# Kernel optimization log

Hardware: AMD Instinct MI355X
Metric: run time of the kernel (lower is better)

Reference implementation:

```python
import jax, jax.numpy as jnp
import numpy as np
import math

HID = 1024   # hidden_dim
QKV = 1024   # qkv_dim
H = 16       # num_heads
DH = QKV // H  # head_dim = 64
BS = 16      # block_size
EPS = 1e-12


def setup_inputs() -> dict:
    key = jax.random.key(0)
    ks = jax.random.split(key, 6)
    B, L = 2, 4096
    s = 0.02
    return {
        "q": jax.random.normal(ks[0], (B, L, HID), jnp.float32),
        "Wq": jax.random.normal(ks[1], (HID, QKV), jnp.float32) * s,
        "Wk": jax.random.normal(ks[2], (HID, QKV), jnp.float32) * s,
        "Wv": jax.random.normal(ks[3], (HID, QKV), jnp.float32) * s,
        "Wo": jax.random.normal(ks[4], (QKV, HID), jnp.float32) * s,
        "bo": jnp.zeros((HID,), jnp.float32),
    }


def _swap_pairs(xb):
    # xb: [B,H,n_blocks,BS,D] -> swap adjacent block pairs along n_blocks
    b, h, n, bs, d = xb.shape
    x = xb.reshape(b, h, n // 2, 2, bs, d)[:, :, :, ::-1]
    return x.reshape(b, h, n, bs, d)


def _block_attend(qb, kb, vb, scale):
    # qb,kb,vb: [B,H,n,BS,D]. Un-normalized block attention (masks are all-ones
    # -> additive mask term is 0). Returns per-block y and row-sum A.
    logits = jnp.einsum('bhnqd,bhnkd->bhnqk', qb * scale, kb)
    logits = logits - jnp.max(logits, axis=-1, keepdims=True)
    A = jnp.exp(logits)
    y = jnp.einsum('bhnqk,bhnkd->bhnqd', A, vb)
    return y, A.sum(axis=-1)


def _to_blocks(x):
    b, h, l, d = x.shape
    return x.reshape(b, h, l // BS, BS, d)


def _forward(q, Wq, Wk, Wv, Wo, bo):
    B, L, _ = q.shape  # L is a power of 2 (4096), no padding needed
    Q, K, V = q @ Wq, q @ Wk, q @ Wv
    sh = lambda x: x.reshape(B, L, H, DH).transpose(0, 2, 1, 3)  # [B,H,L,D]
    Q, K, V = sh(Q), sh(K), sh(V)
    scale = 1.0 / math.sqrt(DH)
    num_levels = int(math.log2(L // BS)) - 1  # 7 for L=4096

    # Multi-level coarsening: avg-pool q/k, sum-pool v (masks all-ones)
    levels = [(Q, K, V)]
    cq, ck, cv = Q, K, V
    for _ in range(num_levels):
        pool = lambda x, red: red(x.reshape(B, H, x.shape[2] // 2, 2, DH), axis=3)
        cq = pool(cq, jnp.mean)
        ck = pool(ck, jnp.mean)
        cv = pool(cv, jnp.sum)
        levels.append((cq, ck, cv))

    # Coarsest-to-finest: block attention against swapped neighbor blocks,
    # repeat-interleave accumulator by 2 at each finer level and add.
    y, A = None, None
    for cq, ck, cv in reversed(levels):
        qb = _to_blocks(cq)
        kb = _swap_pairs(_to_blocks(ck))
        vb = _swap_pairs(_to_blocks(cv))
        yl, Al = _block_attend(qb, kb, vb, scale)
        yl = yl.reshape(B, H, -1, DH)
        Al = Al.reshape(B, H, -1)
        if y is None:
            y, A = yl, Al
        else:
            y = jnp.repeat(y, 2, axis=2) + yl
            A = jnp.repeat(A, 2, axis=2) + Al

    # Finest diagonal blocks, no swap
    yl, Al = _block_attend(_to_blocks(Q), _to_blocks(K), _to_blocks(V), scale)
    y = y + yl.reshape(B, H, L, DH)
    A = A + Al.reshape(B, H, L)

    out = y / (A + EPS)[..., None]
    out = out.transpose(0, 2, 1, 3).reshape(B, L, H * DH)
    return out @ Wo + bo


def reference(q, Wq, Wk, Wv, Wo, bo):
    return _forward(q, Wq, Wk, Wv, Wo, bo)
```

## Files before the change

### kernel.cpp

```cpp
#include <hip/hip_runtime.h>
#include <cstddef>
#include <cstdint>

#define NHEADS 16
#define DHEAD  64
#define SEQL   4096
#define NBH    32
#define PBH_POOL 4064

typedef unsigned short bfu;
typedef unsigned int u32;
typedef __attribute__((ext_vector_type(4)))  float f32x4;
typedef __attribute__((ext_vector_type(16))) float f32x16;
typedef __attribute__((ext_vector_type(8)))  short bf16x8;

__device__ inline float b2f(bfu b) { return __uint_as_float(((unsigned)b) << 16); }
__device__ inline bfu f2b(float f) {
    unsigned u = __float_as_uint(f);
    unsigned r = 0x7FFFu + ((u >> 16) & 1u);
    return (bfu)((u + r) >> 16);
}
__device__ inline u32 pk2(float a, float b) {
    return (u32)f2b(a) | ((u32)f2b(b) << 16);
}
__device__ inline bf16x8 mk8(u32 a, u32 b, u32 c, u32 d) {
    union { u32 u[4]; bf16x8 v; } x;
    x.u[0] = a; x.u[1] = b; x.u[2] = c; x.u[3] = d;
    return x.v;
}

__global__ __launch_bounds__(256) void cvt_q(const float* __restrict__ q, bfu* __restrict__ qb)
{
    size_t g = (size_t)blockIdx.x * 256 + threadIdx.x;
    float4 v = *reinterpret_cast<const float4*>(&q[g * 4]);
    ushort4 s;
    s.x = f2b(v.x); s.y = f2b(v.y); s.z = f2b(v.z); s.w = f2b(v.w);
    *reinterpret_cast<ushort4*>(&qb[g * 4]) = s;
}

__global__ __launch_bounds__(256) void transpose_cvt(
    const float* __restrict__ W0, const float* __restrict__ W1,
    const float* __restrict__ W2, const float* __restrict__ W3,
    bfu* __restrict__ Wt)
{
    __shared__ float t[32][33];
    const int widx = blockIdx.z;
    const float* src = (widx == 0) ? W0 : (widx == 1) ? W1 : (widx == 2) ? W2 : W3;
    bfu* dst = Wt + (size_t)widx * 1048576;
    const int k0 = blockIdx.y * 32, n0 = blockIdx.x * 32;
    const int tx = threadIdx.x & 31, ty = threadIdx.x >> 5;
    #pragma unroll
    for (int i = 0; i < 4; ++i)
        t[ty + 8 * i][tx] = src[(size_t)(k0 + ty + 8 * i) * 1024 + n0 + tx];
    __syncthreads();
    #pragma unroll
    for (int i = 0; i < 4; ++i)
        dst[(size_t)(n0 + ty + 8 * i) * 1024 + k0 + tx] = f2b(t[tx][ty + 8 * i]);
}

template<int MODE>
__global__ __launch_bounds__(256) void gemm_mfma(
    const bfu* __restrict__ A, const bfu* __restrict__ Bt,
    bfu* __restrict__ O0, bfu* __restrict__ O1, bfu* __restrict__ O2,
    float* __restrict__ Ofp, const float* __restrict__ bias)
{
    __shared__ bfu As[128 * 32];
    __shared__ bfu Bs[128 * 32];
    const int tid = threadIdx.x;
    const int lane = tid & 63;
    const int wv = tid >> 6;
    const int wr = wv >> 1, wc = wv & 1;
    const int m0 = blockIdx.y * 128, n0 = blockIdx.x * 128;
    const int rlo = lane & 15, khi = lane >> 4;

    f32x4 acc[4][4];
    #pragma unroll
    for (int i = 0; i < 4; ++i)
        #pragma unroll
        for (int j = 0; j < 4; ++j)
            #pragma unroll
            for (int e = 0; e < 4; ++e) acc[i][j][e] = 0.f;

    for (int kt = 0; kt < 1024; kt += 32) {
        #pragma unroll
        for (int r = 0; r < 2; ++r) {
            int o = (r * 256 + tid) * 16;
            int row = o >> 6;
            int slot = (o >> 4) & 3;
            int sg = slot ^ ((row >> 1) & 3);
            __builtin_amdgcn_global_load_lds(
                (const __attribute__((address_space(1))) u32*)
                    &A[(size_t)(m0 + row) * 1024 + kt + sg * 8],
                (__attribute__((address_space(3))) u32*)
                    (reinterpret_cast<char*>(As) + o), 16, 0, 0);
            __builtin_amdgcn_global_load_lds(
                (const __attribute__((address_space(1))) u32*)
                    &Bt[(size_t)(n0 + row) * 1024 + kt + sg * 8],
                (__attribute__((address_space(3))) u32*)
                    (reinterpret_cast<char*>(Bs) + o), 16, 0, 0);
        }
        __syncthreads();
        bf16x8 af[4], bf_[4];
        #pragma unroll
        for (int mf = 0; mf < 4; ++mf) {
            int row = wr * 64 + mf * 16 + rlo;
            af[mf] = *reinterpret_cast<const bf16x8*>(
                reinterpret_cast<char*>(As) + row * 64 + ((khi ^ ((row >> 1) & 3)) << 4));
        }
        #pragma unroll
        for (int nf = 0; nf < 4; ++nf) {
            int row = wc * 64 + nf * 16 + rlo;
            bf_[nf] = *reinterpret_cast<const bf16x8*>(
                reinterpret_cast<char*>(Bs) + row * 64 + ((khi ^ ((row >> 1) & 3)) << 4));
        }
        #pragma unroll
        for (int mf = 0; mf < 4; ++mf)
            #pragma unroll
            for (int nf = 0; nf < 4; ++nf)
                acc[mf][nf] = __builtin_amdgcn_mfma_f32_16x16x32_bf16(
                    af[mf], bf_[nf], acc[mf][nf], 0, 0, 0);
        __syncthreads();
    }

    if (MODE == 0) {
        #pragma unroll
        for (int mf = 0; mf < 4; ++mf) {
            #pragma unroll
            for (int nf = 0; nf < 4; ++nf) {
                int np = n0 + wc * 64 + nf * 16 + rlo;
                int wsel = np >> 10, n = np & 1023;
                int h = n >> 6, d = n & 63;
                bfu* O = (wsel == 0) ? O0 : ((wsel == 1) ? O1 : O2);
                #pragma unroll
                for (int rr = 0; rr < 4; ++rr) {
                    int m = m0 + wr * 64 + mf * 16 + khi * 4 + rr;
                    int b = m >> 12, l = m & 4095;
                    O[(((size_t)(b * NHEADS + h)) * SEQL + l) * DHEAD + d] = f2b(acc[mf][nf][rr]);
                }
            }
        }
    } else {
        #pragma unroll
        for (int mf = 0; mf < 4; ++mf) {
            #pragma unroll
            for (int nf = 0; nf < 4; ++nf) {
                int np = n0 + wc * 64 + nf * 16 + rlo;
                float bb = bias[np];
                #pragma unroll
                for (int rr = 0; rr < 4; ++rr) {
                    int m = m0 + wr * 64 + mf * 16 + khi * 4 + rr;
                    Ofp[(size_t)m * 1024 + np] = acc[mf][nf][rr] + bb;
                }
            }
        }
    }
}

__global__ __launch_bounds__(256) void transpose_v(
    const bfu* __restrict__ Vb, bfu* __restrict__ Vt0)
{
    __shared__ bfu tile[64 * 64];
    const int bh = blockIdx.y, l0 = blockIdx.x * 64;
    const int t = threadIdx.x;
    const int row = t >> 3, chunk = t & 7;
    #pragma unroll
    for (int it = 0; it < 2; ++it) {
        int r = it * 32 + row;
        uint4 v = *reinterpret_cast<const uint4*>(
            &Vb[((size_t)bh * SEQL + l0 + r) * 64 + chunk * 8]);
        bfu e[8];
        e[0] = v.x & 0xffff; e[1] = v.x >> 16; e[2] = v.y & 0xffff; e[3] = v.y >> 16;
        e[4] = v.z & 0xffff; e[5] = v.z >> 16; e[6] = v.w & 0xffff; e[7] = v.w >> 16;
        int pr = r ^ (chunk * 8);
        #pragma unroll
        for (int j = 0; j < 8; ++j) tile[(chunk * 8 + j) * 64 + pr] = e[j];
    }
    __syncthreads();
    #pragma unroll
    for (int it = 0; it < 2; ++it) {
        int d = it * 32 + (t >> 3);
        int lc = t & 7;
        int plc = lc ^ (d >> 3);
        uint4 v = *reinterpret_cast<const uint4*>(&tile[d * 64 + plc * 8]);
        *reinterpret_cast<uint4*>(
            &Vt0[((size_t)bh * 64 + d) * SEQL + l0 + lc * 8]) = v;
    }
}

__global__ __launch_bounds__(256) void pool2x(
    const bfu* __restrict__ sq, const bfu* __restrict__ sk, const bfu* __restrict__ svt,
    bfu* __restrict__ dq, bfu* __restrict__ dk, bfu* __restrict__ dvt,
    int srcPerBH, int srcRow0, int dstRow0, int dstRows, int svtCols)
{
    int g = blockIdx.x * 256 + threadIdx.x;
    int half = NBH * dstRows * 16;
    if (g < half) {
        int per = dstRows * 16;
        int bh = g / per, f = g % per;
        int r = f >> 4, cc = (f & 15) * 4;
        size_t s0 = ((size_t)bh * srcPerBH + srcRow0 + 2 * r) * 64 + cc;
        size_t di = ((size_t)bh * PBH_POOL + dstRow0 + r) * 64 + cc;
        ushort4 a, b, o;
        a = *reinterpret_cast<const ushort4*>(&sq[s0]);
        b = *reinterpret_cast<const ushort4*>(&sq[s0 + 64]);
        o.x = f2b((b2f(a.x) + b2f(b.x)) * 0.5f);
        o.y = f2b((b2f(a.y) + b2f(b.y)) * 0.5f);
        o.z = f2b((b2f(a.z) + b2f(b.z)) * 0.5f);
        o.w = f2b((b2f(a.w) + b2f(b.w)) * 0.5f);
        *reinterpret_cast<ushort4*>(&dq[di]) = o;
        a = *reinterpret_cast<const ushort4*>(&sk[s0]);
        b = *reinterpret_cast<const ushort4*>(&sk[s0 + 64]);
        o.x = f2b((b2f(a.x) + b2f(b.x)) * 0.5f);
        o.y = f2b((b2f(a.y) + b2f(b.y)) * 0.5f);
        o.z = f2b((b2f(a.z) + b2f(b.z)) * 0.5f);
        o.w = f2b((b2f(a.w) + b2f(b.w)) * 0.5f);
        *reinterpret_cast<ushort4*>(&dk[di]) = o;
    } else {
        g -= half;
        int nr4 = dstRows >> 2;
        int per = 64 * nr4;
        int bh = g / per, f = g % per;
        int d = f / nr4, r4 = (f % nr4) * 4;
        const bfu* srow = svt + ((size_t)bh * 64 + d) * svtCols + srcRow0 + 2 * r4;
        uint4 v = *reinterpret_cast<const uint4*>(srow);
        ushort4 o;
        o.x = f2b(b2f(v.x & 0xffff) + b2f(v.x >> 16));
        o.y = f2b(b2f(v.y & 0xffff) + b2f(v.y >> 16));
        o.z = f2b(b2f(v.z & 0xffff) + b2f(v.z >> 16));
        o.w = f2b(b2f(v.w & 0xffff) + b2f(v.w >> 16));
        *reinterpret_cast<ushort4*>(&dvt[((size_t)bh * 64 + d) * PBH_POOL + dstRow0 + r4]) = o;
    }
}

__global__ __launch_bounds__(64) void pair_attn(
    const bfu* __restrict__ Q0, const bfu* __restrict__ K0, const bfu* __restrict__ Vt0,
    const bfu* __restrict__ Qp, const bfu* __restrict__ Kp, const bfu* __restrict__ Vtp,
    bfu* __restrict__ y0, float* __restrict__ A0,
    bfu* __restrict__ ylev, float* __restrict__ Alev)
{
    const int bh = blockIdx.y;
    int s = blockIdx.x, lvl = 0, cnt = 128;
    while (s >= cnt) { s -= cnt; cnt >>= 1; ++lvl; }
    const bfu *Q, *K, *Vt; int perbh, vcols, loff;
    if (lvl == 0) { Q = Q0; K = K0; Vt = Vt0; perbh = SEQL; vcols = SEQL; loff = 0; }
    else { Q = Qp; K = Kp; Vt = Vtp; perbh = PBH_POOL; vcols = PBH_POOL; loff = 4096 - (8192 >> lvl); }
    const int rbase = loff + s * 32;
    const int t = threadIdx.x, q31 = t & 31, hl = t >> 5;

    const bfu* Krow = K + ((size_t)bh * perbh + rbase + q31) * 64 + hl * 8;
    const bfu* Qrow = Q + ((size_t)bh * perbh + rbase + q31) * 64 + hl * 8;

    f32x16 S;
    #pragma unroll
    for (int e = 0; e < 16; ++e) S[e] = 0.f;
    #pragma unroll
    for (int db = 0; db < 4; ++db) {
        bf16x8 ka = *reinterpret_cast<const bf16x8*>(Krow + db * 16);
        bf16x8 qa = *reinterpret_cast<const bf16x8*>(Qrow + db * 16);
        S = __builtin_amdgcn_mfma_f32_32x32x16_bf16(ka, qa, S, 0, 0, 0);
    }

    float p[16];
    #pragma unroll
    for (int r = 0; r < 16; ++r) p[r] = S[r] * 0.125f;
    float mlo = p[0], mhi = p[8];
    #pragma unroll
    for (int r = 1; r < 8; ++r) { mlo = fmaxf(mlo, p[r]); mhi = fmaxf(mhi, p[r + 8]); }
    mlo = fmaxf(mlo, __shfl_xor(mlo, 32));
    mhi = fmaxf(mhi, __shfl_xor(mhi, 32));
    #pragma unroll
    for (int r = 0; r < 8; ++r) {
        p[r]     = __expf(p[r]     - mlo);
        p[r + 8] = __expf(p[r + 8] - mhi);
    }
    if (lvl > 0) {
        #pragma unroll
        for (int r = 0; r < 8; ++r) {
            if (q31 < 16) p[r] = 0.f; else p[r + 8] = 0.f;
        }
    }
    float alo = 0.f, ahi = 0.f;
    #pragma unroll
    for (int r = 0; r < 8; ++r) { alo += p[r]; ahi += p[r + 8]; }
    alo += __shfl_xor(alo, 32);
    ahi += __shfl_xor(ahi, 32);
    const float Asum = alo + ahi;

    bf16x8 Pop[2];
    #pragma unroll
    for (int m = 0; m < 2; ++m) {
        u32 a0 = pk2(p[8 * m + 0], p[8 * m + 1]);
        u32 a1 = pk2(p[8 * m + 2], p[8 * m + 3]);
        u32 b0 = pk2(p[8 * m + 4], p[8 * m + 5]);
        u32 b1 = pk2(p[8 * m + 6], p[8 * m + 7]);
        u32 pa0 = __shfl_xor(a0, 32), pa1 = __shfl_xor(a1, 32);
        u32 pb0 = __shfl_xor(b0, 32), pb1 = __shfl_xor(b1, 32);
        Pop[m] = (hl == 0) ? mk8(a0, a1, pa0, pa1) : mk8(pb0, pb1, b0, b1);
    }

    const bfu* Vbase = Vt + (size_t)bh * 64 * vcols + rbase + hl * 8;
    f32x16 y[2];
    #pragma unroll
    for (int tt = 0; tt < 2; ++tt) {
        #pragma unroll
        for (int e = 0; e < 16; ++e) y[tt][e] = 0.f;
        #pragma unroll
        for (int m = 0; m < 2; ++m) {
            bf16x8 va = *reinterpret_cast<const bf16x8*>(
                Vbase + (size_t)(tt * 32 + q31) * vcols + m * 16);
            y[tt] = __builtin_amdgcn_mfma_f32_32x32x16_bf16(va, Pop[m], y[tt], 0, 0, 0);
        }
    }

    if (lvl == 0) {
        const int b = bh >> 4, h = bh & 15;
        bfu* orow = y0 + ((size_t)(b * SEQL + rbase + q31)) * 1024 + h * 64;
        #pragma unroll
        for (int tt = 0; tt < 2; ++tt)
            #pragma unroll
            for (int g = 0; g < 4; ++g) {
                int d0 = tt * 32 + g * 8 + hl * 4;
                ushort4 s4;
                s4.x = f2b(y[tt][4 * g + 0]); s4.y = f2b(y[tt][4 * g + 1]);
                s4.z = f2b(y[tt][4 * g + 2]); s4.w = f2b(y[tt][4 * g + 3]);
                *reinterpret_cast<ushort4*>(orow + d0) = s4;
            }
        if (hl == 0) A0[(size_t)bh * SEQL + rbase + q31] = Asum;
    } else {
        bfu* orow = ylev + ((size_t)bh * PBH_POOL + rbase + q31) * 64;
        #pragma unroll
        for (int tt = 0; tt < 2; ++tt)
            #pragma unroll
            for (int g = 0; g < 4; ++g) {
                int d0 = tt * 32 + g * 8 + hl * 4;
                ushort4 s4;
                s4.x = f2b(y[tt][4 * g + 0]); s4.y = f2b(y[tt][4 * g + 1]);
                s4.z = f2b(y[tt][4 * g + 2]); s4.w = f2b(y[tt][4 * g + 3]);
                *reinterpret_cast<ushort4*>(orow + d0) = s4;
            }
        if (hl == 0) Alev[(size_t)bh * PBH_POOL + rbase + q31] = Asum;
    }
}

__global__ __launch_bounds__(256) void gather_norm(
    const bfu* __restrict__ ylev, const float* __restrict__ Alev,
    const float* __restrict__ A0, bfu* __restrict__ y0)
{
    size_t g = (size_t)blockIdx.x * 256 + threadIdx.x;
    int d = (int)(g & 63);
    int h = (int)((g >> 6) & 15);
    int l = (int)((g >> 10) & 4095);
    int b = (int)(g >> 22);
    int bh = b * NHEADS + h;

    float ys = b2f(y0[g]);
    float as = A0[(size_t)bh * SEQL + l];
    #pragma unroll
    for (int lvl = 1; lvl <= 7; ++lvl) {
        int r = (4096 - (8192 >> lvl)) + (l >> lvl);
        ys += b2f(ylev[((size_t)bh * PBH_POOL + r) * 64 + d]);
        as += Alev[(size_t)bh * PBH_POOL + r];
    }
    y0[g] = f2b(ys / (as + 1e-12f));
}

extern "C" void kernel_launch(void* const* d_in, const int* in_sizes, int n_in,
                              void* d_out, int out_size, void* d_ws, size_t ws_size,
                              hipStream_t stream)
{
    const float* q  = (const float*)d_in[0];
    const float* Wq = (const float*)d_in[1];
    const float* Wk = (const float*)d_in[2];
    const float* Wv = (const float*)d_in[3];
    const float* Wo = (const float*)d_in[4];
    const float* bo = (const float*)d_in[5];
    float* out = (float*)d_out;

    const size_t NE0 = (size_t)NBH * SEQL * 64;
    const size_t NEP = (size_t)NBH * PBH_POOL * 64;
    bfu* qb   = (bfu*)d_ws;
    bfu* Wt   = qb + NE0;
    bfu* Qb   = Wt + 4 * 1048576;
    bfu* Kb   = Qb + NE0;
    bfu* Vb   = Kb + NE0;
    bfu* Vt0  = Vb + NE0;
    bfu* Qp   = Vt0 + NE0;
    bfu* Kp   = Qp + NEP;
    bfu* ylev = Kp + NEP;
    float* Alev = (float*)(ylev + NEP);
    float* A0   = Alev + (size_t)NBH * PBH_POOL;
    bfu* Vtp  = Vb;

    cvt_q<<<8192, 256, 0, stream>>>(q, qb);
    transpose_cvt<<<dim3(32, 32, 4), 256, 0, stream>>>(Wq, Wk, Wv, Wo, Wt);

    gemm_mfma<0><<<dim3(24, 64), 256, 0, stream>>>(
        qb, Wt, Qb, Kb, Vb, nullptr, nullptr);

    transpose_v<<<dim3(64, NBH), 256, 0, stream>>>(Vb, Vt0);

    for (int lvl = 1; lvl < 8; ++lvl) {
        int Ld = 4096 >> lvl;
        int srcPerBH = (lvl == 1) ? SEQL : PBH_POOL;
        int srcRow0  = (lvl == 1) ? 0 : (4096 - (8192 >> (lvl - 1)));
        int dstRow0  = 4096 - (8192 >> lvl);
        const bfu* sq  = (lvl == 1) ? Qb : Qp;
        const bfu* sk  = (lvl == 1) ? Kb : Kp;
        const bfu* svt = (lvl == 1) ? Vt0 : Vtp;
        int svtCols    = (lvl == 1) ? SEQL : PBH_POOL;
        int nblk = (NBH * Ld * 32) / 256;
        pool2x<<<nblk, 256, 0, stream>>>(sq, sk, svt, Qp, Kp, Vtp,
                                         srcPerBH, srcRow0, dstRow0, Ld, svtCols);
    }

    pair_attn<<<dim3(255, NBH), 64, 0, stream>>>(
        Qb, Kb, Vt0, Qp, Kp, Vtp, qb , A0, ylev, Alev);

    gather_norm<<<32768, 256, 0, stream>>>(ylev, Alev, A0, qb);

    gemm_mfma<1><<<dim3(8, 64), 256, 0, stream>>>(
        qb, Wt + 3 * 1048576, nullptr, nullptr, nullptr, out, bo);
}
```

Baseline: 288.9 us.

## Fuse prep kernels, write V transposed from GEMM, single-pass pooling, vectorize gather

Merges the q conversion and weight transpose into one launch, and has the QKV GEMM epilogue write V directly in transposed layout, which removes the separate transpose_v kernel. The seven per-level pool launches become one kernel in which each block pools a 128-row segment through all levels in shared memory. pair_attn packs four 64-thread slots into each 256-thread block, and gather_norm handles four elements per thread with vector loads. This cuts launch count and global round-trips. Pooled levels are now computed in fp32 from the finest bf16 data rather than re-rounded at each level, and the pool kernel uses a large shared-memory footprint.

```diff
diff --git a/kernel.cpp b/kernel.cpp
--- a/kernel.cpp
+++ b/kernel.cpp
@@ -29,33 +29,36 @@
     return x.v;
 }
 
-__global__ __launch_bounds__(256) void cvt_q(const float* __restrict__ q, bfu* __restrict__ qb)
-{
-    size_t g = (size_t)blockIdx.x * 256 + threadIdx.x;
-    float4 v = *reinterpret_cast<const float4*>(&q[g * 4]);
-    ushort4 s;
-    s.x = f2b(v.x); s.y = f2b(v.y); s.z = f2b(v.z); s.w = f2b(v.w);
-    *reinterpret_cast<ushort4*>(&qb[g * 4]) = s;
-}
-
-__global__ __launch_bounds__(256) void transpose_cvt(
+__global__ __launch_bounds__(256) void prep(
+    const float* __restrict__ q,
     const float* __restrict__ W0, const float* __restrict__ W1,
     const float* __restrict__ W2, const float* __restrict__ W3,
-    bfu* __restrict__ Wt)
-{
-    __shared__ float t[32][33];
-    const int widx = blockIdx.z;
-    const float* src = (widx == 0) ? W0 : (widx == 1) ? W1 : (widx == 2) ? W2 : W3;
-    bfu* dst = Wt + (size_t)widx * 1048576;
-    const int k0 = blockIdx.y * 32, n0 = blockIdx.x * 32;
-    const int tx = threadIdx.x & 31, ty = threadIdx.x >> 5;
-    #pragma unroll
-    for (int i = 0; i < 4; ++i)
-        t[ty + 8 * i][tx] = src[(size_t)(k0 + ty + 8 * i) * 1024 + n0 + tx];
-    __syncthreads();
-    #pragma unroll
-    for (int i = 0; i < 4; ++i)
-        dst[(size_t)(n0 + ty + 8 * i) * 1024 + k0 + tx] = f2b(t[tx][ty + 8 * i]);
+    bfu* __restrict__ qb, bfu* __restrict__ Wt)
+{
+    const int bid = blockIdx.x;
+    if (bid < 8192) {
+        size_t g = (size_t)bid * 256 + threadIdx.x;
+        float4 v = *reinterpret_cast<const float4*>(&q[g * 4]);
+        ushort4 s;
+        s.x = f2b(v.x); s.y = f2b(v.y); s.z = f2b(v.z); s.w = f2b(v.w);
+        *reinterpret_cast<ushort4*>(&qb[g * 4]) = s;
+    } else {
+        __shared__ float tl[32][33];
+        const int b2 = bid - 8192;
+        const int widx = b2 >> 10;
+        const int tile = b2 & 1023;
+        const float* src = (widx == 0) ? W0 : (widx == 1) ? W1 : (widx == 2) ? W2 : W3;
+        bfu* dst = Wt + (size_t)widx * 1048576;
+        const int n0 = (tile & 31) * 32, k0 = (tile >> 5) * 32;
+        const int tx = threadIdx.x & 31, ty = threadIdx.x >> 5;
+        #pragma unroll
+        for (int i = 0; i < 4; ++i)
+            tl[ty + 8 * i][tx] = src[(size_t)(k0 + ty + 8 * i) * 1024 + n0 + tx];
+        __syncthreads();
+        #pragma unroll
+        for (int i = 0; i < 4; ++i)
+            dst[(size_t)(n0 + ty + 8 * i) * 1024 + k0 + tx] = f2b(tl[tx][ty + 8 * i]);
+    }
 }
 
 template<int MODE>
@@ -125,17 +128,25 @@
     if (MODE == 0) {
         #pragma unroll
         for (int mf = 0; mf < 4; ++mf) {
+            int l0m = m0 + wr * 64 + mf * 16 + khi * 4;
+            int b = l0m >> 12, l0 = l0m & 4095;
             #pragma unroll
             for (int nf = 0; nf < 4; ++nf) {
                 int np = n0 + wc * 64 + nf * 16 + rlo;
                 int wsel = np >> 10, n = np & 1023;
                 int h = n >> 6, d = n & 63;
-                bfu* O = (wsel == 0) ? O0 : ((wsel == 1) ? O1 : O2);
-                #pragma unroll
-                for (int rr = 0; rr < 4; ++rr) {
-                    int m = m0 + wr * 64 + mf * 16 + khi * 4 + rr;
-                    int b = m >> 12, l = m & 4095;
-                    O[(((size_t)(b * NHEADS + h)) * SEQL + l) * DHEAD + d] = f2b(acc[mf][nf][rr]);
+                if (wsel == 2) {
+                    ushort4 s4;
+                    s4.x = f2b(acc[mf][nf][0]); s4.y = f2b(acc[mf][nf][1]);
+                    s4.z = f2b(acc[mf][nf][2]); s4.w = f2b(acc[mf][nf][3]);
+                    *reinterpret_cast<ushort4*>(
+                        &O2[((size_t)(b * NHEADS + h) * 64 + d) * SEQL + l0]) = s4;
+                } else {
+                    bfu* O = (wsel == 0) ? O0 : O1;
+                    #pragma unroll
+                    for (int rr = 0; rr < 4; ++rr)
+                        O[(((size_t)(b * NHEADS + h)) * SEQL + l0 + rr) * DHEAD + d]
+                            = f2b(acc[mf][nf][rr]);
                 }
             }
         }
@@ -156,96 +167,107 @@
     }
 }
 
-__global__ __launch_bounds__(256) void transpose_v(
-    const bfu* __restrict__ Vb, bfu* __restrict__ Vt0)
-{
-    __shared__ bfu tile[64 * 64];
-    const int bh = blockIdx.y, l0 = blockIdx.x * 64;
+__global__ __launch_bounds__(256) void pool_all(
+    const bfu* __restrict__ Qb, const bfu* __restrict__ Kb, const bfu* __restrict__ Vt0,
+    bfu* __restrict__ Qp, bfu* __restrict__ Kp, bfu* __restrict__ Vtp)
+{
+    __shared__ bfu stg[8192];
+    __shared__ float buf0[4096];
+    __shared__ float buf1[4096];
+    const int bid = blockIdx.x;
     const int t = threadIdx.x;
-    const int row = t >> 3, chunk = t & 7;
-    #pragma unroll
-    for (int it = 0; it < 2; ++it) {
-        int r = it * 32 + row;
-        uint4 v = *reinterpret_cast<const uint4*>(
-            &Vb[((size_t)bh * SEQL + l0 + r) * 64 + chunk * 8]);
-        bfu e[8];
-        e[0] = v.x & 0xffff; e[1] = v.x >> 16; e[2] = v.y & 0xffff; e[3] = v.y >> 16;
-        e[4] = v.z & 0xffff; e[5] = v.z >> 16; e[6] = v.w & 0xffff; e[7] = v.w >> 16;
-        int pr = r ^ (chunk * 8);
-        #pragma unroll
-        for (int j = 0; j < 8; ++j) tile[(chunk * 8 + j) * 64 + pr] = e[j];
-    }
-    __syncthreads();
-    #pragma unroll
-    for (int it = 0; it < 2; ++it) {
-        int d = it * 32 + (t >> 3);
-        int lc = t & 7;
-        int plc = lc ^ (d >> 3);
-        uint4 v = *reinterpret_cast<const uint4*>(&tile[d * 64 + plc * 8]);
-        *reinterpret_cast<uint4*>(
-            &Vt0[((size_t)bh * 64 + d) * SEQL + l0 + lc * 8]) = v;
-    }
-}
-
-__global__ __launch_bounds__(256) void pool2x(
-    const bfu* __restrict__ sq, const bfu* __restrict__ sk, const bfu* __restrict__ svt,
-    bfu* __restrict__ dq, bfu* __restrict__ dk, bfu* __restrict__ dvt,
-    int srcPerBH, int srcRow0, int dstRow0, int dstRows, int svtCols)
-{
-    int g = blockIdx.x * 256 + threadIdx.x;
-    int half = NBH * dstRows * 16;
-    if (g < half) {
-        int per = dstRows * 16;
-        int bh = g / per, f = g % per;
-        int r = f >> 4, cc = (f & 15) * 4;
-        size_t s0 = ((size_t)bh * srcPerBH + srcRow0 + 2 * r) * 64 + cc;
-        size_t di = ((size_t)bh * PBH_POOL + dstRow0 + r) * 64 + cc;
-        ushort4 a, b, o;
-        a = *reinterpret_cast<const ushort4*>(&sq[s0]);
-        b = *reinterpret_cast<const ushort4*>(&sq[s0 + 64]);
-        o.x = f2b((b2f(a.x) + b2f(b.x)) * 0.5f);
-        o.y = f2b((b2f(a.y) + b2f(b.y)) * 0.5f);
-        o.z = f2b((b2f(a.z) + b2f(b.z)) * 0.5f);
-        o.w = f2b((b2f(a.w) + b2f(b.w)) * 0.5f);
-        *reinterpret_cast<ushort4*>(&dq[di]) = o;
-        a = *reinterpret_cast<const ushort4*>(&sk[s0]);
-        b = *reinterpret_cast<const ushort4*>(&sk[s0 + 64]);
-        o.x = f2b((b2f(a.x) + b2f(b.x)) * 0.5f);
-        o.y = f2b((b2f(a.y) + b2f(b.y)) * 0.5f);
-        o.z = f2b((b2f(a.z) + b2f(b.z)) * 0.5f);
-        o.w = f2b((b2f(a.w) + b2f(b.w)) * 0.5f);
-        *reinterpret_cast<ushort4*>(&dk[di]) = o;
+
+    if (bid < 2048) {
+        const int tensor = bid >> 10;
+        const int bh = (bid & 1023) >> 5, seg = bid & 31;
+        const bfu* src = (tensor ? Kb : Qb) + ((size_t)bh * SEQL + seg * 128) * 64;
+        bfu* dst = (tensor ? Kp : Qp) + (size_t)bh * PBH_POOL * 64;
+        #pragma unroll
+        for (int it = 0; it < 4; ++it) {
+            int tt = it * 256 + t;
+            *reinterpret_cast<uint4*>(&stg[(tt >> 3) * 64 + (tt & 7) * 8]) =
+                *reinterpret_cast<const uint4*>(&src[(size_t)(tt >> 3) * 64 + (tt & 7) * 8]);
+        }
+        __syncthreads();
+        {
+            int d = t & 63;
+            #pragma unroll
+            for (int i = 0; i < 16; ++i) {
+                int r = (t >> 6) + 4 * i;
+                float v = (b2f(stg[(2 * r) * 64 + d]) + b2f(stg[(2 * r + 1) * 64 + d])) * 0.5f;
+                buf0[r * 64 + d] = v;
+                dst[(size_t)(seg * 64 + r) * 64 + d] = f2b(v);
+            }
+        }
+        __syncthreads();
+        int nr = 32, dstRow0 = 2048;
+        float* cur = buf0; float* nxt = buf1;
+        for (int lvl = 2; lvl <= 7; ++lvl) {
+            int elems = nr * 64;
+            for (int i = t; i < elems; i += 256) {
+                int r = i >> 6, dd = i & 63;
+                float v = (cur[(2 * r) * 64 + dd] + cur[(2 * r + 1) * 64 + dd]) * 0.5f;
+                nxt[r * 64 + dd] = v;
+                dst[(size_t)(dstRow0 + seg * nr + r) * 64 + dd] = f2b(v);
+            }
+            __syncthreads();
+            float* tmp = cur; cur = nxt; nxt = tmp;
+            dstRow0 += 4096 >> lvl;
+            nr >>= 1;
+        }
     } else {
-        g -= half;
-        int nr4 = dstRows >> 2;
-        int per = 64 * nr4;
-        int bh = g / per, f = g % per;
-        int d = f / nr4, r4 = (f % nr4) * 4;
-        const bfu* srow = svt + ((size_t)bh * 64 + d) * svtCols + srcRow0 + 2 * r4;
-        uint4 v = *reinterpret_cast<const uint4*>(srow);
-        ushort4 o;
-        o.x = f2b(b2f(v.x & 0xffff) + b2f(v.x >> 16));
-        o.y = f2b(b2f(v.y & 0xffff) + b2f(v.y >> 16));
-        o.z = f2b(b2f(v.z & 0xffff) + b2f(v.z >> 16));
-        o.w = f2b(b2f(v.w & 0xffff) + b2f(v.w >> 16));
-        *reinterpret_cast<ushort4*>(&dvt[((size_t)bh * 64 + d) * PBH_POOL + dstRow0 + r4]) = o;
-    }
-}
-
-__global__ __launch_bounds__(64) void pair_attn(
+        const int b2 = bid - 2048;
+        const int bh = b2 >> 5, seg = b2 & 31;
+        const bfu* src = Vt0 + (size_t)bh * 64 * SEQL + seg * 128;
+        bfu* dst = Vtp + (size_t)bh * 64 * PBH_POOL;
+        #pragma unroll
+        for (int it = 0; it < 4; ++it) {
+            int tt = it * 256 + t;
+            *reinterpret_cast<uint4*>(&stg[(tt >> 4) * 128 + (tt & 15) * 8]) =
+                *reinterpret_cast<const uint4*>(&src[(size_t)(tt >> 4) * SEQL + (tt & 15) * 8]);
+        }
+        __syncthreads();
+        for (int i = t; i < 4096; i += 256) {
+            int dd = i >> 6, c = i & 63;
+            float v = b2f(stg[dd * 128 + 2 * c]) + b2f(stg[dd * 128 + 2 * c + 1]);
+            buf0[dd * 64 + c] = v;
+            dst[(size_t)dd * PBH_POOL + seg * 64 + c] = f2b(v);
+        }
+        __syncthreads();
+        int nc = 32, lg = 5, dstRow0 = 2048;
+        float* cur = buf0; float* nxt = buf1;
+        for (int lvl = 2; lvl <= 7; ++lvl) {
+            int elems = 64 * nc;
+            for (int i = t; i < elems; i += 256) {
+                int dd = i >> lg, c = i & (nc - 1);
+                float v = cur[dd * 64 + 2 * c] + cur[dd * 64 + 2 * c + 1];
+                nxt[dd * 64 + c] = v;
+                dst[(size_t)dd * PBH_POOL + dstRow0 + seg * nc + c] = f2b(v);
+            }
+            __syncthreads();
+            float* tmp = cur; cur = nxt; nxt = tmp;
+            dstRow0 += 4096 >> lvl;
+            nc >>= 1; --lg;
+        }
+    }
+}
+
+__global__ __launch_bounds__(256) void pair_attn(
     const bfu* __restrict__ Q0, const bfu* __restrict__ K0, const bfu* __restrict__ Vt0,
     const bfu* __restrict__ Qp, const bfu* __restrict__ Kp, const bfu* __restrict__ Vtp,
     bfu* __restrict__ y0, float* __restrict__ A0,
     bfu* __restrict__ ylev, float* __restrict__ Alev)
 {
     const int bh = blockIdx.y;
-    int s = blockIdx.x, lvl = 0, cnt = 128;
+    const int slot = blockIdx.x * 4 + (threadIdx.x >> 6);
+    if (slot >= 255) return;
+    int s = slot, lvl = 0, cnt = 128;
     while (s >= cnt) { s -= cnt; cnt >>= 1; ++lvl; }
     const bfu *Q, *K, *Vt; int perbh, vcols, loff;
     if (lvl == 0) { Q = Q0; K = K0; Vt = Vt0; perbh = SEQL; vcols = SEQL; loff = 0; }
     else { Q = Qp; K = Kp; Vt = Vtp; perbh = PBH_POOL; vcols = PBH_POOL; loff = 4096 - (8192 >> lvl); }
     const int rbase = loff + s * 32;
-    const int t = threadIdx.x, q31 = t & 31, hl = t >> 5;
+    const int t = threadIdx.x & 63, q31 = t & 31, hl = t >> 5;
 
     const bfu* Krow = K + ((size_t)bh * perbh + rbase + q31) * 64 + hl * 8;
     const bfu* Qrow = Q + ((size_t)bh * perbh + rbase + q31) * 64 + hl * 8;
@@ -346,22 +368,28 @@
     const bfu* __restrict__ ylev, const float* __restrict__ Alev,
     const float* __restrict__ A0, bfu* __restrict__ y0)
 {
-    size_t g = (size_t)blockIdx.x * 256 + threadIdx.x;
-    int d = (int)(g & 63);
-    int h = (int)((g >> 6) & 15);
-    int l = (int)((g >> 10) & 4095);
-    int b = (int)(g >> 22);
+    size_t idx = ((size_t)blockIdx.x * 256 + threadIdx.x) * 4;
+    int d0 = (int)(idx & 63);
+    int h = (int)((idx >> 6) & 15);
+    int l = (int)((idx >> 10) & 4095);
+    int b = (int)(idx >> 22);
     int bh = b * NHEADS + h;
 
-    float ys = b2f(y0[g]);
+    ushort4 y4 = *reinterpret_cast<const ushort4*>(&y0[idx]);
+    float ys0 = b2f(y4.x), ys1 = b2f(y4.y), ys2 = b2f(y4.z), ys3 = b2f(y4.w);
     float as = A0[(size_t)bh * SEQL + l];
     #pragma unroll
     for (int lvl = 1; lvl <= 7; ++lvl) {
         int r = (4096 - (8192 >> lvl)) + (l >> lvl);
-        ys += b2f(ylev[((size_t)bh * PBH_POOL + r) * 64 + d]);
+        ushort4 v4 = *reinterpret_cast<const ushort4*>(
+            &ylev[((size_t)bh * PBH_POOL + r) * 64 + d0]);
+        ys0 += b2f(v4.x); ys1 += b2f(v4.y); ys2 += b2f(v4.z); ys3 += b2f(v4.w);
         as += Alev[(size_t)bh * PBH_POOL + r];
     }
-    y0[g] = f2b(ys / (as + 1e-12f));
+    float inv = 1.0f / (as + 1e-12f);
+    ushort4 o;
+    o.x = f2b(ys0 * inv); o.y = f2b(ys1 * inv); o.z = f2b(ys2 * inv); o.w = f2b(ys3 * inv);
+    *reinterpret_cast<ushort4*>(&y0[idx]) = o;
 }
 
 extern "C" void kernel_launch(void* const* d_in, const int* in_sizes, int n_in,
@@ -382,41 +410,25 @@
     bfu* Wt   = qb + NE0;
     bfu* Qb   = Wt + 4 * 1048576;
     bfu* Kb   = Qb + NE0;
-    bfu* Vb   = Kb + NE0;
-    bfu* Vt0  = Vb + NE0;
+    bfu* Vt0  = Kb + NE0;
     bfu* Qp   = Vt0 + NE0;
     bfu* Kp   = Qp + NEP;
-    bfu* ylev = Kp + NEP;
+    bfu* Vtp  = Kp + NEP;
+    bfu* ylev = Vtp + NEP;
     float* Alev = (float*)(ylev + NEP);
     float* A0   = Alev + (size_t)NBH * PBH_POOL;
-    bfu* Vtp  = Vb;
-
-    cvt_q<<<8192, 256, 0, stream>>>(q, qb);
-    transpose_cvt<<<dim3(32, 32, 4), 256, 0, stream>>>(Wq, Wk, Wv, Wo, Wt);
+
+    prep<<<12288, 256, 0, stream>>>(q, Wq, Wk, Wv, Wo, qb, Wt);
 
     gemm_mfma<0><<<dim3(24, 64), 256, 0, stream>>>(
-        qb, Wt, Qb, Kb, Vb, nullptr, nullptr);
-
-    transpose_v<<<dim3(64, NBH), 256, 0, stream>>>(Vb, Vt0);
-
-    for (int lvl = 1; lvl < 8; ++lvl) {
-        int Ld = 4096 >> lvl;
-        int srcPerBH = (lvl == 1) ? SEQL : PBH_POOL;
-        int srcRow0  = (lvl == 1) ? 0 : (4096 - (8192 >> (lvl - 1)));
-        int dstRow0  = 4096 - (8192 >> lvl);
-        const bfu* sq  = (lvl == 1) ? Qb : Qp;
-        const bfu* sk  = (lvl == 1) ? Kb : Kp;
-        const bfu* svt = (lvl == 1) ? Vt0 : Vtp;
-        int svtCols    = (lvl == 1) ? SEQL : PBH_POOL;
-        int nblk = (NBH * Ld * 32) / 256;
-        pool2x<<<nblk, 256, 0, stream>>>(sq, sk, svt, Qp, Kp, Vtp,
-                                         srcPerBH, srcRow0, dstRow0, Ld, svtCols);
-    }
-
-    pair_attn<<<dim3(255, NBH), 64, 0, stream>>>(
+        qb, Wt, Qb, Kb, Vt0, nullptr, nullptr);
+
+    pool_all<<<3072, 256, 0, stream>>>(Qb, Kb, Vt0, Qp, Kp, Vtp);
+
+    pair_attn<<<dim3(64, NBH), 256, 0, stream>>>(
         Qb, Kb, Vt0, Qp, Kp, Vtp, qb , A0, ylev, Alev);
 
-    gather_norm<<<32768, 256, 0, stream>>>(ylev, Alev, A0, qb);
+    gather_norm<<<8192, 256, 0, stream>>>(ylev, Alev, A0, qb);
 
     gemm_mfma<1><<<dim3(8, 64), 256, 0, stream>>>(
         qb, Wt + 3 * 1048576, nullptr, nullptr, nullptr, out, bo);
```

New measurement: 260.6 us. -9.8%, faster.
